# Performance work log

Measured on AMD Instinct MI355X. Metric: run time of the kernel, lower is better.

The kernel has to match this reference:

```python
import jax, jax.numpy as jnp
import numpy as np
import math

PATCH = 32
NBINS = 36
EPS = 1e-18
PI = math.pi


def _sobel_grads(patch):
    # kornia SpatialGradient('sobel', 1, normalized=True): cross-correlation with
    # sobel kernels divided by sum(|k|)=8, replicate padding. out: [B,2,H,W]
    kx = jnp.array([[-1., 0., 1.], [-2., 0., 2.], [-1., 0., 1.]], dtype=patch.dtype) / 8.0
    ky = kx.T
    k = jnp.stack([kx, ky])[:, None]  # [2,1,3,3] OIHW
    p = jnp.pad(patch, ((0, 0), (0, 0), (1, 1), (1, 1)), mode='edge')
    return jax.lax.conv_general_dilated(p, k, (1, 1), 'VALID',
                                        dimension_numbers=('NCHW', 'OIHW', 'NCHW'))


def setup_inputs() -> dict:
    key = jax.random.key(0)
    B = 32768
    patch = jax.random.normal(key, (B, 1, PATCH, PATCH), dtype=jnp.float32)
    # default conf: gauss_weighted=False, circular_kernel=False -> ones kernel
    weight_kernel = jnp.ones((PATCH, PATCH), dtype=jnp.float32)
    # hard-coded circular Conv1d smoothing weights
    smooth_w = jnp.array([0.33, 0.34, 0.33], dtype=jnp.float32)
    return {"patch": patch, "weight_kernel": weight_kernel, "smooth_w": smooth_w}


def reference(patch, weight_kernel, smooth_w):
    B = patch.shape[0]
    HW = PATCH * PATCH
    g = _sobel_grads(patch) * weight_kernel          # [B,2,32,32]
    gx, gy = g[:, 0], g[:, 1]
    mag = jnp.sqrt(gx * gx + gy * gy + EPS)
    ori = jnp.arctan2(gy, gx + EPS) + 2.0 * PI
    # soft binning: linear split of magnitude between two adjacent angular bins
    o_big = NBINS * (ori + PI) / (2.0 * PI)
    bo0f = jnp.floor(o_big)
    w1 = o_big - bo0f
    bo0 = jnp.mod(bo0f, NBINS).astype(jnp.int32)
    bo1 = jnp.mod(bo0 + 1, NBINS)
    wo0 = (1.0 - w1) * mag
    wo1 = w1 * mag
    # fused scatter-histogram (replaces the 36-iteration mask+avg_pool loop);
    # adaptive_avg_pool2d(...,(1,1)) == mean over HW == scatter-sum / HW
    base = (jnp.arange(B, dtype=jnp.int32) * NBINS)[:, None]   # [B,1]
    ids = jnp.concatenate([(base + bo0.reshape(B, HW)).reshape(-1),
                           (base + bo1.reshape(B, HW)).reshape(-1)])
    vals = jnp.concatenate([wo0.reshape(-1), wo1.reshape(-1)])
    hist = jax.ops.segment_sum(vals, ids, num_segments=B * NBINS).reshape(B, NBINS) / HW
    # circular conv1d, kernel size 3, padding 1: out[i] = w0*h[i-1] + w1*h[i] + w2*h[i+1]
    hist_s = (smooth_w[0] * jnp.roll(hist, 1, axis=1)
              + smooth_w[1] * hist
              + smooth_w[2] * jnp.roll(hist, -1, axis=1))
    values = jnp.max(hist_s, axis=1)                 # [B]
    indices = jnp.argmax(hist_s, axis=1)             # [B]
    ip1 = jnp.mod(indices + 1, NBINS)
    im1 = jnp.mod(indices - 1, NBINS)
    vp1 = jnp.take_along_axis(hist_s, ip1[:, None], axis=1)[:, 0]
    vm1 = jnp.take_along_axis(hist_s, im1[:, None], axis=1)[:, 0]
    # parabolic sub-bin refinement (conf['ref']=False branch)
    refinement = (vp1 - vm1) / 2.0 / (2.0 * values - (vp1 + vm1))
    idx_ref = indices.astype(patch.dtype) + refinement
    angle = -(2.0 * PI * idx_ref / float(NBINS) - PI)  # conf['refined']=True
    return angle
```

## Files before the change

### kernel.cpp

```cpp
#include <hip/hip_runtime.h>
#include <math.h>

#define PATCH   32
#define NBINS   36
#define WPB     4
#define HW_N    (PATCH*PATCH)


__global__ __launch_bounds__(256, 4) void patch_dom_orient_kernel(
    const float* __restrict__ patch,
    const float* __restrict__ wk,
    const float* __restrict__ sw,
    float* __restrict__ out,
    int num_patches)
{
    __shared__ float  tile[WPB][PATCH][PATCH + 1];
    __shared__ double hist[WPB][NBINS];
    __shared__ double hsm [WPB][NBINS];
    __shared__ double ctab[37];
    __shared__ double stab[37];

    const int tid  = threadIdx.x;
    const int w    = tid >> 6;
    const int lane = tid & 63;
    const int p    = blockIdx.x * WPB + w;
    const int pc   = (p < num_patches) ? p : (num_patches - 1);

    if (lane < NBINS) hist[w][lane] = 0.0;
    if (tid < 37) {
        double a = ((double)tid - 18.0) * 0.17453292519943295;
        ctab[tid] = cos(a);
        stab[tid] = sin(a);
    }

    const float4* pp4 = reinterpret_cast<const float4*>(patch + (size_t)pc * HW_N);
    #pragma unroll
    for (int i = 0; i < 4; ++i) {
        int idx4 = i * 64 + lane;
        float4 v = pp4[idx4];
        int flat = idx4 * 4;
        int row = flat >> 5;
        int col = flat & 31;
        tile[w][row][col + 0] = v.x;
        tile[w][row][col + 1] = v.y;
        tile[w][row][col + 2] = v.z;
        tile[w][row][col + 3] = v.w;
    }
    __syncthreads();

    for (int i = 0; i < HW_N / 64; ++i) {
        int idx = i * 64 + lane;
        int y = idx >> 5, x = idx & 31;
        int ym = (y == 0) ? 0 : y - 1;
        int yp = (y == PATCH - 1) ? PATCH - 1 : y + 1;
        int xm = (x == 0) ? 0 : x - 1;
        int xp = (x == PATCH - 1) ? PATCH - 1 : x + 1;

        double pmm = (double)tile[w][ym][xm], pm0 = (double)tile[w][ym][x], pmp = (double)tile[w][ym][xp];
        double p0m = (double)tile[w][y ][xm],                               p0p = (double)tile[w][y ][xp];
        double ppm = (double)tile[w][yp][xm], pp0 = (double)tile[w][yp][x], ppp = (double)tile[w][yp][xp];

        double wf = (double)wk[idx] * 0.125;
        double gx = ((pmp + 2.0 * p0p + ppp) - (pmm + 2.0 * p0m + ppm)) * wf;
        double gy = ((ppm + 2.0 * pp0 + ppp) - (pmm + 2.0 * pm0 + pmp)) * wf;

        double m2  = fma(gx, gx, fma(gy, gy, 1e-18));
        double inv = rsqrt(m2);
        double mag = m2 * inv;
        double xs  = gx + 1e-18;

        float xf = (float)xs, yf = (float)gy;
        float ax = fabsf(xf), ay = fabsf(yf);
        float mn = fminf(ax, ay), mx = fmaxf(ax, ay);
        float r  = mn * __builtin_amdgcn_rcpf(mx);
        float s2 = r * r;
        float at = r * fmaf(s2, fmaf(s2, 0.0792f, -0.2885f), 0.9954f);
        if (ay > ax)    at = 1.5707963f - at;
        if (xf < 0.0f)  at = 3.1415927f - at;
        at = copysignf(at, yf);
        int n = (int)rintf(at * 5.7295780f);

        double c  = ctab[n + 18];
        double s  = stab[n + 18];
        double yr = fma(gy, c, -(xs * s));
        double z  = yr * inv;
        double u  = z * z;
        double dl = z * fma(u, fma(u, fma(u, fma(u, 35.0/1152.0, 5.0/112.0),
                                          3.0/40.0), 1.0/6.0), 1.0);
        double phi = fma(dl, 5.729577951308232, (double)n);
        double fl  = floor(phi);
        double w1  = phi - fl;
        int bh = 54 + (int)fl;
        int b0 = bh % 36;
        int b1 = b0 + 1; if (b1 >= 36) b1 = 0;

        double wo1 = w1 * mag;
        atomicAdd(&hist[w][b0], (1.0 - w1) * mag);
        atomicAdd(&hist[w][b1], wo1);
    }
    __syncthreads();

    double hs_val = -INFINITY;
    if (lane < NBINS) {
        int im1 = (lane == 0) ? NBINS - 1 : lane - 1;
        int ip1 = (lane == NBINS - 1) ? 0 : lane + 1;
        double hm = hist[w][im1] * (1.0 / 1024.0);
        double h0 = hist[w][lane] * (1.0 / 1024.0);
        double hp = hist[w][ip1] * (1.0 / 1024.0);
        hs_val = (double)sw[0] * hm + (double)sw[1] * h0 + (double)sw[2] * hp;
        hsm[w][lane] = hs_val;
    }
    __syncthreads();

    double v  = hs_val;
    int    bi = (lane < NBINS) ? lane : 64;
    #pragma unroll
    for (int sft = 32; sft > 0; sft >>= 1) {
        double ov = __shfl_xor(v, sft, 64);
        int    oi = __shfl_xor(bi, sft, 64);
        if (ov > v || (ov == v && oi < bi)) { v = ov; bi = oi; }
    }

    if (lane == 0 && p < num_patches) {
        int ip = (bi == NBINS - 1) ? 0 : bi + 1;
        int im = (bi == 0) ? NBINS - 1 : bi - 1;
        double vp1 = hsm[w][ip];
        double vm1 = hsm[w][im];
        double refinement = ((vp1 - vm1) / 2.0) / (2.0 * v - (vp1 + vm1));
        double idx_ref = (double)bi + refinement;
        double angle = -((2.0 * M_PI * idx_ref) / 36.0 - M_PI);
        out[p] = (float)angle;
    }
}

extern "C" void kernel_launch(void* const* d_in, const int* in_sizes, int n_in,
                              void* d_out, int out_size, void* d_ws, size_t ws_size,
                              hipStream_t stream) {
    const float* patch = (const float*)d_in[0];
    const float* wk    = (const float*)d_in[1];
    const float* sw    = (const float*)d_in[2];
    float* out = (float*)d_out;

    int num_patches = in_sizes[0] / HW_N;
    int blocks = (num_patches + WPB - 1) / WPB;

    patch_dom_orient_kernel<<<blocks, 256, 0, stream>>>(patch, wk, sw, out, num_patches);
}
```

Baseline: 259.8 us.

## Use double padded halo tile, privatized histograms, float rsqrt with Newton step

Stores the patch in shared memory as doubles with a one-pixel replicated halo, which removes the edge-clamp index math and the per-tap float-to-double conversions. The weight kernel is staged into shared memory once, pre-scaled by 0.125. Each warp now keeps two histogram copies selected by lane parity, which is meant to halve double-atomic contention. The double rsqrt is replaced by a float rsqrt plus one Newton step, and the bin index is clamped. The larger shared footprint lowers occupancy, and launch_bounds is reduced to 2 to match.

```diff
diff --git a/kernel.cpp b/kernel.cpp
--- a/kernel.cpp
+++ b/kernel.cpp
@@ -5,17 +5,20 @@
 #define NBINS   36
 #define WPB     4
 #define HW_N    (PATCH*PATCH)
+#define TR      34
+#define TC      35
 
 
-__global__ __launch_bounds__(256, 4) void patch_dom_orient_kernel(
+__global__ __launch_bounds__(256, 2) void patch_dom_orient_kernel(
     const float* __restrict__ patch,
     const float* __restrict__ wk,
     const float* __restrict__ sw,
     float* __restrict__ out,
     int num_patches)
 {
-    __shared__ float  tile[WPB][PATCH][PATCH + 1];
-    __shared__ double hist[WPB][NBINS];
+    __shared__ double tile[WPB][TR][TC];
+    __shared__ double wkl[HW_N];
+    __shared__ double hist[WPB][2][NBINS];
     __shared__ double hsm [WPB][NBINS];
     __shared__ double ctab[37];
     __shared__ double stab[37];
@@ -26,13 +29,24 @@
     const int p    = blockIdx.x * WPB + w;
     const int pc   = (p < num_patches) ? p : (num_patches - 1);
 
-    if (lane < NBINS) hist[w][lane] = 0.0;
+    {
+        double* hf = &hist[w][0][0];
+        hf[lane] = 0.0;
+        if (lane < 8) hf[64 + lane] = 0.0;
+    }
     if (tid < 37) {
         double a = ((double)tid - 18.0) * 0.17453292519943295;
         ctab[tid] = cos(a);
         stab[tid] = sin(a);
     }
-
+    {
+        float4 v = reinterpret_cast<const float4*>(wk)[tid];
+        double* dst = &wkl[tid * 4];
+        dst[0] = (double)v.x * 0.125;
+        dst[1] = (double)v.y * 0.125;
+        dst[2] = (double)v.z * 0.125;
+        dst[3] = (double)v.w * 0.125;
+    }
     const float4* pp4 = reinterpret_cast<const float4*>(patch + (size_t)pc * HW_N);
     #pragma unroll
     for (int i = 0; i < 4; ++i) {
@@ -41,62 +55,80 @@
         int flat = idx4 * 4;
         int row = flat >> 5;
         int col = flat & 31;
-        tile[w][row][col + 0] = v.x;
-        tile[w][row][col + 1] = v.y;
-        tile[w][row][col + 2] = v.z;
-        tile[w][row][col + 3] = v.w;
+        double* dst = &tile[w][row + 1][col + 1];
+        dst[0] = (double)v.x;
+        dst[1] = (double)v.y;
+        dst[2] = (double)v.z;
+        dst[3] = (double)v.w;
     }
+    {
+        int r = (lane >> 1) + 1;
+        if (lane & 1) tile[w][r][33] = tile[w][r][32];
+        else          tile[w][r][0]  = tile[w][r][1];
+    }
+    if (lane < 34) tile[w][0][lane]  = tile[w][1][lane];
+    if (lane < 34) tile[w][33][lane] = tile[w][32][lane];
     __syncthreads();
 
+    #pragma unroll 2
     for (int i = 0; i < HW_N / 64; ++i) {
         int idx = i * 64 + lane;
         int y = idx >> 5, x = idx & 31;
-        int ym = (y == 0) ? 0 : y - 1;
-        int yp = (y == PATCH - 1) ? PATCH - 1 : y + 1;
-        int xm = (x == 0) ? 0 : x - 1;
-        int xp = (x == PATCH - 1) ? PATCH - 1 : x + 1;
+        const double* c0 = &tile[w][y + 1][x + 1];
 
-        double pmm = (double)tile[w][ym][xm], pm0 = (double)tile[w][ym][x], pmp = (double)tile[w][ym][xp];
-        double p0m = (double)tile[w][y ][xm],                               p0p = (double)tile[w][y ][xp];
-        double ppm = (double)tile[w][yp][xm], pp0 = (double)tile[w][yp][x], ppp = (double)tile[w][yp][xp];
+        double pmm = c0[-TC - 1], pm0 = c0[-TC], pmp = c0[-TC + 1];
+        double p0m = c0[-1],                     p0p = c0[1];
+        double ppm = c0[ TC - 1], pp0 = c0[ TC], ppp = c0[ TC + 1];
+        double wf  = wkl[idx];
 
-        double wf = (double)wk[idx] * 0.125;
-        double gx = ((pmp + 2.0 * p0p + ppp) - (pmm + 2.0 * p0m + ppm)) * wf;
-        double gy = ((ppm + 2.0 * pp0 + ppp) - (pmm + 2.0 * pm0 + pmp)) * wf;
+        double d1 = pmp - pmm, d2 = p0p - p0m, d3 = ppp - ppm;
+        double gx = (fma(d2, 2.0, d1) + d3) * wf;
+        double e1 = ppm - pmm, e2 = pp0 - pm0, e3 = ppp - pmp;
+        double gy = (fma(e2, 2.0, e1) + e3) * wf;
 
-        double m2  = fma(gx, gx, fma(gy, gy, 1e-18));
-        double inv = rsqrt(m2);
-        double mag = m2 * inv;
-        double xs  = gx + 1e-18;
+        double xs = gx + 1e-18;
+        double m2 = fma(gx, gx, fma(gy, gy, 1e-18));
+
+        float  rf = rsqrtf((float)m2);
+        double r0 = (double)rf;
+        double tt = r0 * r0;
+        double hm = m2 * 0.5;
+        double r  = r0 * fma(-hm, tt, 1.5);
+        double mag = m2 * r;
 
         float xf = (float)xs, yf = (float)gy;
         float ax = fabsf(xf), ay = fabsf(yf);
         float mn = fminf(ax, ay), mx = fmaxf(ax, ay);
-        float r  = mn * __builtin_amdgcn_rcpf(mx);
-        float s2 = r * r;
-        float at = r * fmaf(s2, fmaf(s2, 0.0792f, -0.2885f), 0.9954f);
-        if (ay > ax)    at = 1.5707963f - at;
-        if (xf < 0.0f)  at = 3.1415927f - at;
+        float rr = mn * __builtin_amdgcn_rcpf(mx);
+        float s2 = rr * rr;
+        float at = rr * fmaf(s2, fmaf(s2, 0.0792f, -0.2885f), 0.9954f);
+        if (ay > ax)   at = 1.5707963f - at;
+        if (xf < 0.0f) at = 3.1415927f - at;
         at = copysignf(at, yf);
         int n = (int)rintf(at * 5.7295780f);
+        n = (n < -18) ? -18 : ((n > 18) ? 18 : n);
 
-        double c  = ctab[n + 18];
-        double s  = stab[n + 18];
-        double yr = fma(gy, c, -(xs * s));
-        double z  = yr * inv;
+        double cn = ctab[n + 18];
+        double sn = stab[n + 18];
+        double yr = fma(gy, cn, -(xs * sn));
+        double z  = yr * r;
         double u  = z * z;
-        double dl = z * fma(u, fma(u, fma(u, fma(u, 35.0/1152.0, 5.0/112.0),
-                                          3.0/40.0), 1.0/6.0), 1.0);
+        double dl = z * fma(u, fma(u, fma(u, fma(u, 35.0 / 1152.0, 5.0 / 112.0),
+                                          3.0 / 40.0), 1.0 / 6.0), 1.0);
         double phi = fma(dl, 5.729577951308232, (double)n);
         double fl  = floor(phi);
         double w1  = phi - fl;
+
         int bh = 54 + (int)fl;
-        int b0 = bh % 36;
-        int b1 = b0 + 1; if (b1 >= 36) b1 = 0;
+        int b0 = bh - ((bh >= 36) ? 36 : 0);
+        b0 = (b0 < 0) ? 0 : ((b0 > 35) ? 35 : b0);
+        int b1 = (b0 == 35) ? 0 : b0 + 1;
 
         double wo1 = w1 * mag;
-        atomicAdd(&hist[w][b0], (1.0 - w1) * mag);
-        atomicAdd(&hist[w][b1], wo1);
+        double wo0 = mag - wo1;
+        int rep = lane & 1;
+        atomicAdd(&hist[w][rep][b0], wo0);
+        atomicAdd(&hist[w][rep][b1], wo1);
     }
     __syncthreads();
 
@@ -104,10 +136,11 @@
     if (lane < NBINS) {
         int im1 = (lane == 0) ? NBINS - 1 : lane - 1;
         int ip1 = (lane == NBINS - 1) ? 0 : lane + 1;
-        double hm = hist[w][im1] * (1.0 / 1024.0);
-        double h0 = hist[w][lane] * (1.0 / 1024.0);
-        double hp = hist[w][ip1] * (1.0 / 1024.0);
-        hs_val = (double)sw[0] * hm + (double)sw[1] * h0 + (double)sw[2] * hp;
+        double hm = hist[w][0][im1]  + hist[w][1][im1];
+        double h0 = hist[w][0][lane] + hist[w][1][lane];
+        double hp = hist[w][0][ip1]  + hist[w][1][ip1];
+        hs_val = ((double)sw[0] * hm + (double)sw[1] * h0 + (double)sw[2] * hp)
+                 * (1.0 / 1024.0);
         hsm[w][lane] = hs_val;
     }
     __syncthreads();
```

Measured after the change: 274.5 us. 1.06x slower.
